# Optimization experiments

Measured on AMD Instinct MI355X. Metric: run time of the kernel, lower is better.

## Reference

```python
import jax, jax.numpy as jnp
import numpy as np

D_MODEL = 1024
N_HEADS = 16
D_FF = 4096
HEAD_DIM = D_MODEL // N_HEADS
LN_EPS = 1e-5


def layer_norm(x, g, b):
    m = jnp.mean(x, axis=-1, keepdims=True)
    v = jnp.mean(jnp.square(x - m), axis=-1, keepdims=True)
    return (x - m) * jax.lax.rsqrt(v + LN_EPS) * g + b


def setup_inputs() -> dict:
    key = jax.random.key(0)
    ks = jax.random.split(key, 16)
    s = 0.02
    d = {
        'x': jax.random.normal(ks[0], (4, 2048, D_MODEL), jnp.float32),
        'Wq': jax.random.normal(ks[1], (D_MODEL, D_MODEL), jnp.float32) * s,
        'bq': jnp.zeros((D_MODEL,), jnp.float32),
        'Wk': jax.random.normal(ks[2], (D_MODEL, D_MODEL), jnp.float32) * s,
        'bk': jnp.zeros((D_MODEL,), jnp.float32),
        'Wv': jax.random.normal(ks[3], (D_MODEL, D_MODEL), jnp.float32) * s,
        'bv': jnp.zeros((D_MODEL,), jnp.float32),
        'Wo': jax.random.normal(ks[4], (D_MODEL, D_MODEL), jnp.float32) * s,
        'bo': jnp.zeros((D_MODEL,), jnp.float32),
        'W1': jax.random.normal(ks[5], (D_FF, D_MODEL), jnp.float32) * s,
        'b1': jnp.zeros((D_FF,), jnp.float32),
        'W2': jax.random.normal(ks[6], (D_MODEL, D_FF), jnp.float32) * s,
        'b2': jnp.zeros((D_MODEL,), jnp.float32),
        'g1': jnp.ones((D_MODEL,), jnp.float32),
        'be1': jnp.zeros((D_MODEL,), jnp.float32),
        'g2': jnp.ones((D_MODEL,), jnp.float32),
        'be2': jnp.zeros((D_MODEL,), jnp.float32),
    }
    return d


def reference(x, Wq, bq, Wk, bk, Wv, bv, Wo, bo, W1, b1, W2, b2, g1, be1, g2, be2):
    B, S, D = x.shape
    H, hd = N_HEADS, HEAD_DIM
    # QKV projections; chunk along d_model -> heads (same as reshape last dim)
    q = (x @ Wq.T + bq).reshape(B, S, H, hd)
    k = (x @ Wk.T + bk).reshape(B, S, H, hd)
    v = (x @ Wv.T + bv).reshape(B, S, H, hd)
    # scaled dot-product attention (no mask, dropout = identity in eval)
    scores = jnp.einsum('bqhd,bkhd->bhqk', q, k) / jnp.sqrt(jnp.float32(hd))
    attn = jax.nn.softmax(scores, axis=-1)
    ctx = jnp.einsum('bhqk,bkhd->bqhd', attn, v).reshape(B, S, D)
    out1 = ctx @ Wo.T + bo
    out = layer_norm(x + out1, g1, be1)
    out2 = jax.nn.relu(out @ W1.T + b1) @ W2.T + b2
    # NOTE: faithful to source bug: second residual uses out1, not out
    return layer_norm(out1 + out2, g2, be2)
```

## Files before the change

kernel.cpp:

```cpp
#include <hip/hip_runtime.h>

typedef __bf16 bf16_t;
typedef __bf16 bf16x8 __attribute__((ext_vector_type(8)));
typedef __bf16 bf16x4 __attribute__((ext_vector_type(4)));
typedef float  f32x4  __attribute__((ext_vector_type(4)));

#define SEQ   2048
#define DMODEL 1024
#define DFF   4096
#define NHEAD 16
#define HDIM  64
#define MTOK  8192

#define QSCALE 0.18033688f
#define THR_LOG2 11.5f

#define MB (size_t)(1024*1024)
static const size_t XB_OFF   = 0;
static const size_t Q_OFF    = 16*MB;
static const size_t K_OFF    = 32*MB;
static const size_t VT_OFF   = 48*MB;
static const size_t FFN1_OFF = 0;
static const size_t CTX_OFF  = 64*MB;
static const size_t OUT1_OFF = 80*MB;
static const size_t LN1_OFF  = 112*MB;
static const size_t WQKV_OFF = 128*MB;
static const size_t WO_OFF   = 134*MB;
static const size_t W1_OFF   = 136*MB;
static const size_t W2_OFF   = 144*MB;

__device__ inline void gload16(const void* g, void* l) {
    __builtin_amdgcn_global_load_lds((__attribute__((address_space(1))) void*)g,
                                     (__attribute__((address_space(3))) void*)l, 16, 0, 0);
}

__global__ __launch_bounds__(256) void cast_bf16_k(const float* __restrict__ s,
                                                   bf16_t* __restrict__ d, int n8) {
    int i = blockIdx.x * 256 + threadIdx.x;
    if (i >= n8) return;
    float4 v0 = ((const float4*)s)[2*i];
    float4 v1 = ((const float4*)s)[2*i+1];
    bf16x8 o;
    o[0]=(bf16_t)v0.x; o[1]=(bf16_t)v0.y; o[2]=(bf16_t)v0.z; o[3]=(bf16_t)v0.w;
    o[4]=(bf16_t)v1.x; o[5]=(bf16_t)v1.y; o[6]=(bf16_t)v1.z; o[7]=(bf16_t)v1.w;
    *(bf16x8*)(d + (size_t)i*8) = o;
}

__global__ __launch_bounds__(256) void concat_bias_k(const float* __restrict__ a,
                                                     const float* __restrict__ b,
                                                     const float* __restrict__ c,
                                                     float* __restrict__ o) {
    int i = blockIdx.x * 256 + threadIdx.x;
    o[i] = (i < 1024) ? a[i] : ((i < 2048) ? b[i - 1024] : c[i - 2048]);
}

template<int EPI>
__global__ __launch_bounds__(256, 2) void gemm_bt(
    const bf16_t* __restrict__ A, const bf16_t* __restrict__ Bm,
    const float* __restrict__ bias, void* __restrict__ out,
    const float* __restrict__ aux, int M, int N, int K, float scale)
{
    __shared__ bf16_t As[128*64];
    __shared__ bf16_t Bs[128*64];
    const int tid = threadIdx.x;
    const int l   = tid & 63;
    const int wid = tid >> 6;
    const int wm  = wid >> 1, wn = wid & 1;
    const int c16 = l & 15,   g  = l >> 4;
    int lin = blockIdx.y * gridDim.x + blockIdx.x;
    int nwg = gridDim.x * gridDim.y;
    int swz = (lin & 7) * (nwg >> 3) + (lin >> 3);
    const long brow = (long)(swz / gridDim.x) * 128;
    const long bcol = (long)(swz % gridDim.x) * 128;

    f32x4 acc[4][4] = {};

    const int nkt = K >> 6;
    for (int kt = 0; kt < nkt; ++kt) {
        __syncthreads();
        const bf16_t* Ag = A  + brow * K + kt*64;
        const bf16_t* Bg = Bm + bcol * K + kt*64;
#pragma unroll
        for (int c = 0; c < 4; ++c) {
            int e   = (c*256 + tid) * 8;
            int row = e >> 6;
            int col = e & 63;
            gload16(Ag + (long)row*K + col, &As[e]);
            gload16(Bg + (long)row*K + col, &Bs[e]);
        }
        __syncthreads();
#pragma unroll
        for (int kk = 0; kk < 2; ++kk) {
            bf16x8 af[4], bfr[4];
#pragma unroll
            for (int mi = 0; mi < 4; ++mi)
                af[mi] = *(const bf16x8*)&As[(wm*64 + mi*16 + c16)*64 + kk*32 + 8*g];
#pragma unroll
            for (int ni = 0; ni < 4; ++ni)
                bfr[ni] = *(const bf16x8*)&Bs[(wn*64 + ni*16 + c16)*64 + kk*32 + 8*g];
#pragma unroll
            for (int mi = 0; mi < 4; ++mi)
#pragma unroll
                for (int ni = 0; ni < 4; ++ni)
                    acc[mi][ni] = __builtin_amdgcn_mfma_f32_16x16x32_bf16(
                        af[mi], bfr[ni], acc[mi][ni], 0, 0, 0);
        }
    }

#pragma unroll
    for (int ni = 0; ni < 4; ++ni) {
        const long c = bcol + wn*64 + ni*16 + c16;
        const float bv = bias[c];
#pragma unroll
        for (int mi = 0; mi < 4; ++mi) {
#pragma unroll
            for (int i = 0; i < 4; ++i) {
                const long r = brow + wm*64 + mi*16 + g*4 + i;
                float v = (acc[mi][ni][i] + bv) * scale;
                if constexpr (EPI == 2) {
                    ((float*)out)[r*N + c] = v;
                } else {
                    ((float*)out)[r*N + c] = v + aux[r*N + c];
                }
            }
        }
    }
}

template<int EPI>
__global__ __launch_bounds__(512, 2) void gemm256(
    const bf16_t* __restrict__ A, const bf16_t* __restrict__ Bm,
    const float* __restrict__ bias, void* __restrict__ out,
    void* __restrict__ out_k, void* __restrict__ out_v,
    int M, int N, int K)
{
    __shared__ alignas(16) char lds[131072];
    const int tid = threadIdx.x;
    const int l   = tid & 63;
    const int wid = tid >> 6;
    const int wm  = wid >> 2, wn = wid & 3;
    const int c16 = l & 15,   g  = l >> 4;
    const int xsw = (c16 & 7) << 4;

    int lin = blockIdx.y * gridDim.x + blockIdx.x;
    int nwg = gridDim.x * gridDim.y;
    int swz = (lin & 7) * (nwg >> 3) + (lin >> 3);
    const long brow = (long)(swz / gridDim.x) * 256;
    const long bcol = (long)(swz % gridDim.x) * 256;

    const int rowloc = tid >> 3;
    const int srcblk = (tid & 7) ^ ((tid >> 3) & 7);
    const bf16_t* Asrc = A  + (brow + rowloc) * (long)K + srcblk * 8;
    const bf16_t* Bsrc = Bm + (bcol + rowloc) * (long)K + srcblk * 8;

    f32x4 acc[8][4] = {};
    const int NKT = K >> 6;

    auto stA = [&](int cur, int t, int j) {
        gload16(Asrc + (long)j*64*K + (long)t*64, lds + cur*65536 + j*8192 + tid*16);
    };
    auto stB = [&](int cur, int t, int j) {
        gload16(Bsrc + (long)j*64*K + (long)t*64, lds + cur*65536 + 32768 + j*8192 + tid*16);
    };

#pragma unroll
    for (int j = 0; j < 4; ++j) stA(0, 0, j);
#pragma unroll
    for (int j = 0; j < 4; ++j) stB(0, 0, j);
#pragma unroll
    for (int j = 0; j < 4; ++j) stA(1, 1, j);
#pragma unroll
    for (int j = 0; j < 4; ++j) stB(1, 1, j);
    asm volatile("s_waitcnt vmcnt(8)" ::: "memory");
    __builtin_amdgcn_sched_barrier(0);
    __builtin_amdgcn_s_barrier();

    int cur = 0;
    for (int t = 0; t < NKT; ++t, cur ^= 1) {
        const char* aL = lds + cur*65536;
        const char* bL = aL + 32768;
        const bool stg = (t + 2 < NKT);
        bf16x8 a0[4][2], a1[4][2], b0[2][2], b1[2][2];

#pragma unroll
        for (int mi = 0; mi < 4; ++mi)
#pragma unroll
            for (int kk = 0; kk < 2; ++kk)
                a0[mi][kk] = *(const bf16x8*)(aL + (wm*128 + mi*16 + c16)*128 + ((kk*64 + 16*g) ^ xsw));
#pragma unroll
        for (int ni = 0; ni < 2; ++ni)
#pragma unroll
            for (int kk = 0; kk < 2; ++kk)
                b0[ni][kk] = *(const bf16x8*)(bL + (wn*64 + ni*16 + c16)*128 + ((kk*64 + 16*g) ^ xsw));
        __builtin_amdgcn_s_barrier();
        asm volatile("s_waitcnt lgkmcnt(0)" ::: "memory");
        __builtin_amdgcn_sched_barrier(0);
        __builtin_amdgcn_s_setprio(1);
#pragma unroll
        for (int mi = 0; mi < 4; ++mi)
#pragma unroll
            for (int ni = 0; ni < 2; ++ni)
#pragma unroll
                for (int kk = 0; kk < 2; ++kk)
                    acc[mi][ni] = __builtin_amdgcn_mfma_f32_16x16x32_bf16(a0[mi][kk], b0[ni][kk], acc[mi][ni], 0, 0, 0);
        __builtin_amdgcn_s_setprio(0);
        __builtin_amdgcn_s_barrier();

#pragma unroll
        for (int ni = 0; ni < 2; ++ni)
#pragma unroll
            for (int kk = 0; kk < 2; ++kk)
                b1[ni][kk] = *(const bf16x8*)(bL + (wn*64 + (ni+2)*16 + c16)*128 + ((kk*64 + 16*g) ^ xsw));
        if (stg) { stA(cur, t+2, 0); stA(cur, t+2, 2); }
        __builtin_amdgcn_s_barrier();
        asm volatile("s_waitcnt lgkmcnt(0)" ::: "memory");
        __builtin_amdgcn_sched_barrier(0);
        __builtin_amdgcn_s_setprio(1);
#pragma unroll
        for (int mi = 0; mi < 4; ++mi)
#pragma unroll
            for (int ni = 0; ni < 2; ++ni)
#pragma unroll
                for (int kk = 0; kk < 2; ++kk)
                    acc[mi][ni+2] = __builtin_amdgcn_mfma_f32_16x16x32_bf16(a0[mi][kk], b1[ni][kk], acc[mi][ni+2], 0, 0, 0);
        __builtin_amdgcn_s_setprio(0);
        __builtin_amdgcn_s_barrier();

#pragma unroll
        for (int mi = 0; mi < 4; ++mi)
#pragma unroll
            for (int kk = 0; kk < 2; ++kk)
                a1[mi][kk] = *(const bf16x8*)(aL + (wm*128 + (mi+4)*16 + c16)*128 + ((kk*64 + 16*g) ^ xsw));
        if (stg) { stB(cur, t+2, 0); stB(cur, t+2, 1); }
        __builtin_amdgcn_s_barrier();
        asm volatile("s_waitcnt lgkmcnt(0)" ::: "memory");
        __builtin_amdgcn_sched_barrier(0);
        __builtin_amdgcn_s_setprio(1);
#pragma unroll
        for (int mi = 0; mi < 4; ++mi)
#pragma unroll
            for (int ni = 0; ni < 2; ++ni)
#pragma unroll
                for (int kk = 0; kk < 2; ++kk)
                    acc[mi+4][ni] = __builtin_amdgcn_mfma_f32_16x16x32_bf16(a1[mi][kk], b0[ni][kk], acc[mi+4][ni], 0, 0, 0);
        __builtin_amdgcn_s_setprio(0);
        __builtin_amdgcn_s_barrier();

        if (stg) { stA(cur, t+2, 1); stA(cur, t+2, 3); stB(cur, t+2, 2); stB(cur, t+2, 3); }
        __builtin_amdgcn_s_barrier();
        __builtin_amdgcn_s_setprio(1);
#pragma unroll
        for (int mi = 0; mi < 4; ++mi)
#pragma unroll
            for (int ni = 0; ni < 2; ++ni)
#pragma unroll
                for (int kk = 0; kk < 2; ++kk)
                    acc[mi+4][ni+2] = __builtin_amdgcn_mfma_f32_16x16x32_bf16(a1[mi][kk], b1[ni][kk], acc[mi+4][ni+2], 0, 0, 0);
        __builtin_amdgcn_s_setprio(0);
        if (stg)                asm volatile("s_waitcnt vmcnt(8)" ::: "memory");
        else if (t < NKT - 1)   asm volatile("s_waitcnt vmcnt(0)" ::: "memory");
        __builtin_amdgcn_sched_barrier(0);
        __builtin_amdgcn_s_barrier();
    }

#pragma unroll
    for (int ni = 0; ni < 4; ++ni) {
        const long c = bcol + wn*64 + ni*16 + c16;
        const float bv = bias[c];
#pragma unroll
        for (int mi = 0; mi < 8; ++mi) {
#pragma unroll
            for (int i = 0; i < 4; ++i) {
                const long r = brow + wm*128 + mi*16 + g*4 + i;
                float v = acc[mi][ni][i] + bv;
                if constexpr (EPI == 3) {
                    ((bf16_t*)out)[r*N + c] = (bf16_t)fmaxf(v, 0.f);
                } else {
                    const int mat = (int)(c >> 10);
                    const int hc  = (int)(c & 1023);
                    const long bb = r >> 11, sidx = r & (SEQ-1);
                    const long hb = bb*NHEAD + (hc >> 6);
                    if (mat == 0)
                        ((bf16_t*)out)[(hb*SEQ + sidx)*HDIM + (hc & 63)] = (bf16_t)(v * QSCALE);
                    else if (mat == 1)
                        ((bf16_t*)out_k)[(hb*SEQ + sidx)*HDIM + (hc & 63)] = (bf16_t)v;
                    else
                        ((bf16_t*)out_v)[(hb*HDIM + (hc & 63))*SEQ + sidx] = (bf16_t)v;
                }
            }
        }
    }
}

__device__ __forceinline__ void kload(bf16x8 (&dst)[4][2], const bf16_t* kb0,
                                      int ktt, int c16, int g) {
    const bf16_t* kbase = kb0 + (size_t)ktt*64*HDIM;
#pragma unroll
    for (int jk = 0; jk < 4; ++jk)
#pragma unroll
        for (int ks = 0; ks < 2; ++ks)
            dst[jk][ks] = *(const bf16x8*)(kbase + (size_t)(16*jk + c16)*HDIM + ks*32 + 8*g);
}

__device__ __forceinline__ void vload(bf16x8 (&vr)[4][2], const bf16_t* vt0,
                                      int ktt, int c16, int g) {
#pragma unroll
    for (int nf = 0; nf < 4; ++nf)
#pragma unroll
        for (int ks = 0; ks < 2; ++ks)
            vr[nf][ks] = *(const bf16x8*)(vt0 + (size_t)(16*nf + c16)*SEQ + ktt*64 + ks*32 + 8*g);
}

__device__ __forceinline__ void qk_step(f32x4 (&s)[2][4], const bf16x8 (&kr)[4][2],
                                        const bf16x8 (&aq)[2][2]) {
    const f32x4 z = {0.f, 0.f, 0.f, 0.f};
    __builtin_amdgcn_s_setprio(1);
#pragma unroll
    for (int qf = 0; qf < 2; ++qf)
#pragma unroll
        for (int jk = 0; jk < 4; ++jk) {
            s[qf][jk] = __builtin_amdgcn_mfma_f32_16x16x32_bf16(kr[jk][0], aq[qf][0], z, 0, 0, 0);
            s[qf][jk] = __builtin_amdgcn_mfma_f32_16x16x32_bf16(kr[jk][1], aq[qf][1], s[qf][jk], 0, 0, 0);
        }
    __builtin_amdgcn_s_setprio(0);
}

__device__ __forceinline__ void sm_step(f32x4 (&s)[2][4], f32x4 (&acc)[2][4],
                                        float (&m)[2], float (&ls)[2], int g) {
#pragma unroll
    for (int qf = 0; qf < 2; ++qf) {
        f32x4 t01, t23, t03;
#pragma unroll
        for (int i = 0; i < 4; ++i) {
            t01[i] = fmaxf(s[qf][0][i], s[qf][1][i]);
            t23[i] = fmaxf(s[qf][2][i], s[qf][3][i]);
        }
#pragma unroll
        for (int i = 0; i < 4; ++i) t03[i] = fmaxf(t01[i], t23[i]);
        float lmax = fmaxf(fmaxf(t03[0], t03[1]), fmaxf(t03[2], t03[3]));
        if (__any(lmax > m[qf] + THR_LOG2)) {
            float pm = lmax;
            pm = fmaxf(pm, __shfl_xor(pm, 16, 64));
            pm = fmaxf(pm, __shfl_xor(pm, 32, 64));
            float mn   = fmaxf(m[qf], pm);
            float corr = __builtin_exp2f(m[qf] - mn);
            ls[qf] *= corr;
            m[qf]   = mn;
            float c0 = __shfl(corr, 4*g + 0, 64);
            float c1 = __shfl(corr, 4*g + 1, 64);
            float c2 = __shfl(corr, 4*g + 2, 64);
            float c3 = __shfl(corr, 4*g + 3, 64);
#pragma unroll
            for (int nf = 0; nf < 4; ++nf) {
                acc[qf][nf][0] *= c0; acc[qf][nf][1] *= c1;
                acc[qf][nf][2] *= c2; acc[qf][nf][3] *= c3;
            }
        }
#pragma unroll
        for (int jk = 0; jk < 4; ++jk)
#pragma unroll
            for (int i = 0; i < 4; ++i)
                s[qf][jk][i] = __builtin_exp2f(s[qf][jk][i] - m[qf]);
        f32x4 r01, r23, r;
#pragma unroll
        for (int i = 0; i < 4; ++i) {
            r01[i] = s[qf][0][i] + s[qf][1][i];
            r23[i] = s[qf][2][i] + s[qf][3][i];
        }
#pragma unroll
        for (int i = 0; i < 4; ++i) r[i] = r01[i] + r23[i];
        ls[qf] += (r[0] + r[1]) + (r[2] + r[3]);
    }
}

__device__ __forceinline__ void pwrite_step(const f32x4 (&s)[2][4], char* buf, int c16, int g) {
#pragma unroll
    for (int qf = 0; qf < 2; ++qf)
#pragma unroll
        for (int jk = 0; jk < 4; ++jk) {
            bf16x4 pk;
            pk[0]=(bf16_t)s[qf][jk][0]; pk[1]=(bf16_t)s[qf][jk][1];
            pk[2]=(bf16_t)s[qf][jk][2]; pk[3]=(bf16_t)s[qf][jk][3];
            *(bf16x4*)(buf + (qf*16 + c16)*128 + ((32*jk + 8*g) ^ ((c16 & 7) << 4))) = pk;
        }
}

__device__ __forceinline__ void pv_step(f32x4 (&acc)[2][4], const bf16x8 (&vr)[4][2],
                                        const char* buf, int c16, int g) {
    __builtin_amdgcn_s_setprio(1);
#pragma unroll
    for (int qf = 0; qf < 2; ++qf)
#pragma unroll
        for (int ks = 0; ks < 2; ++ks) {
            bf16x8 pa = *(const bf16x8*)(buf + (qf*16 + c16)*128 + ((ks*64 + 16*g) ^ ((c16 & 7) << 4)));
#pragma unroll
            for (int nf = 0; nf < 4; ++nf)
                acc[qf][nf] = __builtin_amdgcn_mfma_f32_16x16x32_bf16(pa, vr[nf][ks], acc[qf][nf], 0, 0, 0);
        }
    __builtin_amdgcn_s_setprio(0);
}

__global__ __launch_bounds__(256, 2) void attn_k(
    const bf16_t* __restrict__ qb, const bf16_t* __restrict__ kb,
    const bf16_t* __restrict__ vt, bf16_t* __restrict__ ctx)
{
    const int id  = blockIdx.x;
    const int idx = id >> 3;
    const int bh  = (id & 7) + 8 * (idx & 7);
    const int qt  = idx >> 3;
    const int w   = threadIdx.x >> 6;
    const int l   = threadIdx.x & 63;
    const int c16 = l & 15, g = l >> 4;
    const int q0  = qt*128 + w*32;

    __shared__ char Ps[4*8192];
    char* myP = &Ps[w*8192];

    bf16x8 aq[2][2];
#pragma unroll
    for (int qf = 0; qf < 2; ++qf) {
        const bf16_t* qrow = qb + ((size_t)bh*SEQ + q0 + qf*16 + c16)*HDIM;
        aq[qf][0] = *(const bf16x8*)(qrow + 8*g);
        aq[qf][1] = *(const bf16x8*)(qrow + 32 + 8*g);
    }

    const bf16_t* kb0 = kb + (size_t)bh*SEQ*HDIM;
    const bf16_t* vt0 = vt + (size_t)bh*HDIM*SEQ;

    f32x4 acc[2][4] = {};
    float m[2]  = {-1e30f, -1e30f};
    float ls[2] = {0.f, 0.f};

    bf16x8 kA[4][2], kB[4][2], vA[4][2], vB[4][2];
    f32x4 s[2][4];

    kload(kA, kb0, 0, c16, g);
    vload(vA, vt0, 0, c16, g);
    kload(kB, kb0, 1, c16, g);
    qk_step(s, kA, aq);
    sm_step(s, acc, m, ls, g);
    pwrite_step(s, myP, c16, g);

    const int NT = SEQ/64;
    for (int t = 0; t < NT - 2; t += 2) {
        qk_step(s, kB, aq);
        asm volatile("s_waitcnt lgkmcnt(0)" ::: "memory");
        __builtin_amdgcn_sched_barrier(0);
        kload(kA, kb0, t + 2, c16, g);
        vload(vB, vt0, t + 1, c16, g);
        __builtin_amdgcn_sched_barrier(0);
        pv_step(acc, vA, myP, c16, g);
        sm_step(s, acc, m, ls, g);
        pwrite_step(s, myP + 4096, c16, g);
        qk_step(s, kA, aq);
        asm volatile("s_waitcnt lgkmcnt(0)" ::: "memory");
        __builtin_amdgcn_sched_barrier(0);
        kload(kB, kb0, t + 3, c16, g);
        vload(vA, vt0, t + 2, c16, g);
        __builtin_amdgcn_sched_barrier(0);
        pv_step(acc, vB, myP + 4096, c16, g);
        sm_step(s, acc, m, ls, g);
        pwrite_step(s, myP, c16, g);
    }
    qk_step(s, kB, aq);
    asm volatile("s_waitcnt lgkmcnt(0)" ::: "memory");
    __builtin_amdgcn_sched_barrier(0);
    vload(vB, vt0, NT - 1, c16, g);
    __builtin_amdgcn_sched_barrier(0);
    pv_step(acc, vA, myP, c16, g);
    sm_step(s, acc, m, ls, g);
    pwrite_step(s, myP + 4096, c16, g);
    asm volatile("s_waitcnt lgkmcnt(0)" ::: "memory");
    __builtin_amdgcn_sched_barrier(0);
    pv_step(acc, vB, myP + 4096, c16, g);

    const int b = bh >> 4, h = bh & 15;
#pragma unroll
    for (int qf = 0; qf < 2; ++qf) {
        float lst = ls[qf];
        lst += __shfl_xor(lst, 16, 64);
        lst += __shfl_xor(lst, 32, 64);
        float i0 = 1.0f / __shfl(lst, 4*g + 0, 64);
        float i1 = 1.0f / __shfl(lst, 4*g + 1, 64);
        float i2 = 1.0f / __shfl(lst, 4*g + 2, 64);
        float i3 = 1.0f / __shfl(lst, 4*g + 3, 64);
#pragma unroll
        for (int nf = 0; nf < 4; ++nf) {
            long col = (size_t)h*HDIM + nf*16 + c16;
            long rb  = (size_t)b*SEQ + q0 + qf*16 + 4*g;
            ctx[(rb + 0)*DMODEL + col] = (bf16_t)(acc[qf][nf][0] * i0);
            ctx[(rb + 1)*DMODEL + col] = (bf16_t)(acc[qf][nf][1] * i1);
            ctx[(rb + 2)*DMODEL + col] = (bf16_t)(acc[qf][nf][2] * i2);
            ctx[(rb + 3)*DMODEL + col] = (bf16_t)(acc[qf][nf][3] * i3);
        }
    }
}

__global__ __launch_bounds__(256) void ln_k(
    const float* __restrict__ a, const float* __restrict__ b,
    const float* __restrict__ g, const float* __restrict__ be,
    float* __restrict__ of, bf16_t* __restrict__ ob)
{
    const long row = blockIdx.x;
    const int tid = threadIdx.x;
    float4 v = ((const float4*)(a + row*DMODEL))[tid];
    if (b) {
        float4 u = ((const float4*)(b + row*DMODEL))[tid];
        v.x += u.x; v.y += u.y; v.z += u.z; v.w += u.w;
    }
    float s = v.x + v.y + v.z + v.w;
    float q = v.x*v.x + v.y*v.y + v.z*v.z + v.w*v.w;
#pragma unroll
    for (int msk = 1; msk < 64; msk <<= 1) {
        s += __shfl_xor(s, msk, 64);
        q += __shfl_xor(q, msk, 64);
    }
    __shared__ float sb[4], qb2[4];
    int w = tid >> 6, lid = tid & 63;
    if (lid == 0) { sb[w] = s; qb2[w] = q; }
    __syncthreads();
    s = sb[0] + sb[1] + sb[2] + sb[3];
    q = qb2[0] + qb2[1] + qb2[2] + qb2[3];
    float mean = s * (1.f/1024.f);
    float var  = q * (1.f/1024.f) - mean*mean;
    float rs   = rsqrtf(var + 1e-5f);
    float4 gv = ((const float4*)g)[tid];
    float4 bv = ((const float4*)be)[tid];
    float o0 = (v.x-mean)*rs*gv.x + bv.x;
    float o1 = (v.y-mean)*rs*gv.y + bv.y;
    float o2 = (v.z-mean)*rs*gv.z + bv.z;
    float o3 = (v.w-mean)*rs*gv.w + bv.w;
    if (ob) {
        bf16x4 o; o[0]=(bf16_t)o0; o[1]=(bf16_t)o1; o[2]=(bf16_t)o2; o[3]=(bf16_t)o3;
        *(bf16x4*)(ob + row*DMODEL + tid*4) = o;
    } else {
        float4 o = make_float4(o0, o1, o2, o3);
        ((float4*)(of + row*DMODEL))[tid] = o;
    }
}

extern "C" void kernel_launch(void* const* d_in, const int* in_sizes, int n_in,
                              void* d_out, int out_size, void* d_ws, size_t ws_size,
                              hipStream_t stream)
{
    const float* x   = (const float*)d_in[0];
    const float* Wq  = (const float*)d_in[1];
    const float* bq  = (const float*)d_in[2];
    const float* Wk  = (const float*)d_in[3];
    const float* bk  = (const float*)d_in[4];
    const float* Wv  = (const float*)d_in[5];
    const float* bvv = (const float*)d_in[6];
    const float* Wo  = (const float*)d_in[7];
    const float* bo  = (const float*)d_in[8];
    const float* W1  = (const float*)d_in[9];
    const float* b1  = (const float*)d_in[10];
    const float* W2  = (const float*)d_in[11];
    const float* b2  = (const float*)d_in[12];
    const float* g1  = (const float*)d_in[13];
    const float* be1 = (const float*)d_in[14];
    const float* g2  = (const float*)d_in[15];
    const float* be2 = (const float*)d_in[16];

    char* ws = (char*)d_ws;
    bf16_t* xb   = (bf16_t*)(ws + XB_OFF);
    bf16_t* qbuf = (bf16_t*)(ws + Q_OFF);
    bf16_t* kbuf = (bf16_t*)(ws + K_OFF);
    bf16_t* vtb  = (bf16_t*)(ws + VT_OFF);
    bf16_t* ffn1 = (bf16_t*)(ws + FFN1_OFF);
    bf16_t* ctxb = (bf16_t*)(ws + CTX_OFF);
    float*  out1 = (float*)(ws + OUT1_OFF);
    bf16_t* ln1b = (bf16_t*)(ws + LN1_OFF);
    bf16_t* wqkv = (bf16_t*)(ws + WQKV_OFF);
    bf16_t* wob  = (bf16_t*)(ws + WO_OFF);
    bf16_t* w1b  = (bf16_t*)(ws + W1_OFF);
    bf16_t* w2b  = (bf16_t*)(ws + W2_OFF);
    float*  biasc= (float*)(ws + OUT1_OFF);
    float*  dout = (float*)d_out;

    auto cast = [&](const float* s, bf16_t* d, long n) {
        int n8 = (int)(n / 8);
        cast_bf16_k<<<(n8 + 255)/256, 256, 0, stream>>>(s, d, n8);
    };
    cast(x,  xb,  (long)MTOK*DMODEL);
    cast(Wq, wqkv,                        (long)DMODEL*DMODEL);
    cast(Wk, wqkv + (long)DMODEL*DMODEL,  (long)DMODEL*DMODEL);
    cast(Wv, wqkv + 2L*DMODEL*DMODEL,     (long)DMODEL*DMODEL);
    cast(Wo, wob, (long)DMODEL*DMODEL);
    cast(W1, w1b, (long)DFF*DMODEL);
    cast(W2, w2b, (long)DMODEL*DFF);
    concat_bias_k<<<12, 256, 0, stream>>>(bq, bk, bvv, biasc);

    gemm256<5><<<dim3(3*DMODEL/256, MTOK/256), dim3(512), 0, stream>>>(
        xb, wqkv, biasc, qbuf, kbuf, vtb, MTOK, 3*DMODEL, DMODEL);
    attn_k<<<dim3((SEQ/128) * 4*NHEAD), dim3(256), 0, stream>>>(qbuf, kbuf, vtb, ctxb);
    gemm_bt<2><<<dim3(DMODEL/128, MTOK/128), dim3(256), 0, stream>>>(
        ctxb, wob, bo, out1, nullptr, MTOK, DMODEL, DMODEL, 1.f);
    ln_k<<<MTOK, dim3(256), 0, stream>>>(x, out1, g1, be1, nullptr, ln1b);
    gemm256<3><<<dim3(DFF/256, MTOK/256), dim3(512), 0, stream>>>(
        ln1b, w1b, b1, ffn1, nullptr, nullptr, MTOK, DFF, DMODEL);
    gemm_bt<4><<<dim3(DMODEL/128, MTOK/128), dim3(256), 0, stream>>>(
        ffn1, w2b, b2, out1, out1, MTOK, DMODEL, DFF, 1.f);
    ln_k<<<MTOK, dim3(256), 0, stream>>>(out1, nullptr, g2, be2, dout, nullptr);
}
```

Measured before the change: 601.8 us.

## Double attention query tile per wave and restructure K/V pipeline per fragment

Each wave now processes 64 query rows, split into four 16-row fragments, instead of 32. The grid is halved to 512 blocks and the P scratch buffer in shared memory is doubled. Each loaded K/V tile is now reused across more queries, cutting global K/V traffic per query. The two-stage software pipeline with A/B register sets is replaced by a single-tile loop that interleaves per-fragment QK, softmax and P writes, and prefetches the next K tile during the last fragment. The costs are more accumulator registers, 64KB of LDS per block that may lower occupancy, fewer blocks to fill the CUs, and less overlap than the old double-buffered scheme.

```diff
diff --git a/kernel.cpp b/kernel.cpp
--- a/kernel.cpp
+++ b/kernel.cpp
@@ -311,92 +311,83 @@
             vr[nf][ks] = *(const bf16x8*)(vt0 + (size_t)(16*nf + c16)*SEQ + ktt*64 + ks*32 + 8*g);
 }
 
-__device__ __forceinline__ void qk_step(f32x4 (&s)[2][4], const bf16x8 (&kr)[4][2],
-                                        const bf16x8 (&aq)[2][2]) {
+__device__ __forceinline__ void qk1(f32x4 (&s)[4], const bf16x8 (&kr)[4][2],
+                                    const bf16x8 (&aqf)[2]) {
     const f32x4 z = {0.f, 0.f, 0.f, 0.f};
     __builtin_amdgcn_s_setprio(1);
 #pragma unroll
-    for (int qf = 0; qf < 2; ++qf)
-#pragma unroll
-        for (int jk = 0; jk < 4; ++jk) {
-            s[qf][jk] = __builtin_amdgcn_mfma_f32_16x16x32_bf16(kr[jk][0], aq[qf][0], z, 0, 0, 0);
-            s[qf][jk] = __builtin_amdgcn_mfma_f32_16x16x32_bf16(kr[jk][1], aq[qf][1], s[qf][jk], 0, 0, 0);
+    for (int jk = 0; jk < 4; ++jk) {
+        s[jk] = __builtin_amdgcn_mfma_f32_16x16x32_bf16(kr[jk][0], aqf[0], z, 0, 0, 0);
+        s[jk] = __builtin_amdgcn_mfma_f32_16x16x32_bf16(kr[jk][1], aqf[1], s[jk], 0, 0, 0);
+    }
+    __builtin_amdgcn_s_setprio(0);
+}
+
+__device__ __forceinline__ void sm1(f32x4 (&s)[4], f32x4 (&accf)[4],
+                                    float& m, float& ls, int g) {
+    f32x4 t01, t23, t03;
+#pragma unroll
+    for (int i = 0; i < 4; ++i) {
+        t01[i] = fmaxf(s[0][i], s[1][i]);
+        t23[i] = fmaxf(s[2][i], s[3][i]);
+    }
+#pragma unroll
+    for (int i = 0; i < 4; ++i) t03[i] = fmaxf(t01[i], t23[i]);
+    float lmax = fmaxf(fmaxf(t03[0], t03[1]), fmaxf(t03[2], t03[3]));
+    if (__any(lmax > m + THR_LOG2)) {
+        float pm = lmax;
+        pm = fmaxf(pm, __shfl_xor(pm, 16, 64));
+        pm = fmaxf(pm, __shfl_xor(pm, 32, 64));
+        float mn   = fmaxf(m, pm);
+        float corr = __builtin_exp2f(m - mn);
+        ls *= corr;
+        m   = mn;
+        float c0 = __shfl(corr, 4*g + 0, 64);
+        float c1 = __shfl(corr, 4*g + 1, 64);
+        float c2 = __shfl(corr, 4*g + 2, 64);
+        float c3 = __shfl(corr, 4*g + 3, 64);
+#pragma unroll
+        for (int nf = 0; nf < 4; ++nf) {
+            accf[nf][0] *= c0; accf[nf][1] *= c1;
+            accf[nf][2] *= c2; accf[nf][3] *= c3;
         }
-    __builtin_amdgcn_s_setprio(0);
-}
-
-__device__ __forceinline__ void sm_step(f32x4 (&s)[2][4], f32x4 (&acc)[2][4],
-                                        float (&m)[2], float (&ls)[2], int g) {
-#pragma unroll
-    for (int qf = 0; qf < 2; ++qf) {
-        f32x4 t01, t23, t03;
-#pragma unroll
-        for (int i = 0; i < 4; ++i) {
-            t01[i] = fmaxf(s[qf][0][i], s[qf][1][i]);
-            t23[i] = fmaxf(s[qf][2][i], s[qf][3][i]);
-        }
-#pragma unroll
-        for (int i = 0; i < 4; ++i) t03[i] = fmaxf(t01[i], t23[i]);
-        float lmax = fmaxf(fmaxf(t03[0], t03[1]), fmaxf(t03[2], t03[3]));
-        if (__any(lmax > m[qf] + THR_LOG2)) {
-            float pm = lmax;
-            pm = fmaxf(pm, __shfl_xor(pm, 16, 64));
-            pm = fmaxf(pm, __shfl_xor(pm, 32, 64));
-            float mn   = fmaxf(m[qf], pm);
-            float corr = __builtin_exp2f(m[qf] - mn);
-            ls[qf] *= corr;
-            m[qf]   = mn;
-            float c0 = __shfl(corr, 4*g + 0, 64);
-            float c1 = __shfl(corr, 4*g + 1, 64);
-            float c2 = __shfl(corr, 4*g + 2, 64);
-            float c3 = __shfl(corr, 4*g + 3, 64);
-#pragma unroll
-            for (int nf = 0; nf < 4; ++nf) {
-                acc[qf][nf][0] *= c0; acc[qf][nf][1] *= c1;
-                acc[qf][nf][2] *= c2; acc[qf][nf][3] *= c3;
-            }
-        }
-#pragma unroll
-        for (int jk = 0; jk < 4; ++jk)
-#pragma unroll
-            for (int i = 0; i < 4; ++i)
-                s[qf][jk][i] = __builtin_exp2f(s[qf][jk][i] - m[qf]);
-        f32x4 r01, r23, r;
-#pragma unroll
-        for (int i = 0; i < 4; ++i) {
-            r01[i] = s[qf][0][i] + s[qf][1][i];
-            r23[i] = s[qf][2][i] + s[qf][3][i];
-        }
-#pragma unroll
-        for (int i = 0; i < 4; ++i) r[i] = r01[i] + r23[i];
-        ls[qf] += (r[0] + r[1]) + (r[2] + r[3]);
-    }
-}
-
-__device__ __forceinline__ void pwrite_step(const f32x4 (&s)[2][4], char* buf, int c16, int g) {
-#pragma unroll
-    for (int qf = 0; qf < 2; ++qf)
-#pragma unroll
-        for (int jk = 0; jk < 4; ++jk) {
-            bf16x4 pk;
-            pk[0]=(bf16_t)s[qf][jk][0]; pk[1]=(bf16_t)s[qf][jk][1];
-            pk[2]=(bf16_t)s[qf][jk][2]; pk[3]=(bf16_t)s[qf][jk][3];
-            *(bf16x4*)(buf + (qf*16 + c16)*128 + ((32*jk + 8*g) ^ ((c16 & 7) << 4))) = pk;
-        }
-}
-
-__device__ __forceinline__ void pv_step(f32x4 (&acc)[2][4], const bf16x8 (&vr)[4][2],
-                                        const char* buf, int c16, int g) {
+    }
+#pragma unroll
+    for (int jk = 0; jk < 4; ++jk)
+#pragma unroll
+        for (int i = 0; i < 4; ++i)
+            s[jk][i] = __builtin_exp2f(s[jk][i] - m);
+    f32x4 r01, r23, r;
+#pragma unroll
+    for (int i = 0; i < 4; ++i) {
+        r01[i] = s[0][i] + s[1][i];
+        r23[i] = s[2][i] + s[3][i];
+    }
+#pragma unroll
+    for (int i = 0; i < 4; ++i) r[i] = r01[i] + r23[i];
+    ls += (r[0] + r[1]) + (r[2] + r[3]);
+}
+
+__device__ __forceinline__ void pw1(const f32x4 (&s)[4], char* buf, int qf, int c16, int g) {
+#pragma unroll
+    for (int jk = 0; jk < 4; ++jk) {
+        bf16x4 pk;
+        pk[0]=(bf16_t)s[jk][0]; pk[1]=(bf16_t)s[jk][1];
+        pk[2]=(bf16_t)s[jk][2]; pk[3]=(bf16_t)s[jk][3];
+        *(bf16x4*)(buf + (qf*16 + c16)*128 + ((32*jk + 8*g) ^ ((c16 & 7) << 4))) = pk;
+    }
+}
+
+__device__ __forceinline__ void pv1(f32x4 (&accf)[4], const bf16x8 (&vr)[4][2],
+                                    const char* buf, int qf, int c16, int g) {
     __builtin_amdgcn_s_setprio(1);
 #pragma unroll
-    for (int qf = 0; qf < 2; ++qf)
-#pragma unroll
-        for (int ks = 0; ks < 2; ++ks) {
-            bf16x8 pa = *(const bf16x8*)(buf + (qf*16 + c16)*128 + ((ks*64 + 16*g) ^ ((c16 & 7) << 4)));
-#pragma unroll
-            for (int nf = 0; nf < 4; ++nf)
-                acc[qf][nf] = __builtin_amdgcn_mfma_f32_16x16x32_bf16(pa, vr[nf][ks], acc[qf][nf], 0, 0, 0);
-        }
+    for (int ks = 0; ks < 2; ++ks) {
+        bf16x8 pa = *(const bf16x8*)(buf + (qf*16 + c16)*128 + ((ks*64 + 16*g) ^ ((c16 & 7) << 4)));
+#pragma unroll
+        for (int nf = 0; nf < 4; ++nf)
+            accf[nf] = __builtin_amdgcn_mfma_f32_16x16x32_bf16(pa, vr[nf][ks], accf[nf], 0, 0, 0);
+    }
     __builtin_amdgcn_s_setprio(0);
 }
 
@@ -411,14 +402,14 @@
     const int w   = threadIdx.x >> 6;
     const int l   = threadIdx.x & 63;
     const int c16 = l & 15, g = l >> 4;
-    const int q0  = qt*128 + w*32;
-
-    __shared__ char Ps[4*8192];
-    char* myP = &Ps[w*8192];
-
-    bf16x8 aq[2][2];
-#pragma unroll
-    for (int qf = 0; qf < 2; ++qf) {
+    const int q0  = qt*256 + w*64;
+
+    __shared__ char Ps[4*16384];
+    char* myP = &Ps[w*16384];
+
+    bf16x8 aq[4][2];
+#pragma unroll
+    for (int qf = 0; qf < 4; ++qf) {
         const bf16_t* qrow = qb + ((size_t)bh*SEQ + q0 + qf*16 + c16)*HDIM;
         aq[qf][0] = *(const bf16x8*)(qrow + 8*g);
         aq[qf][1] = *(const bf16x8*)(qrow + 32 + 8*g);
@@ -427,56 +418,38 @@
     const bf16_t* kb0 = kb + (size_t)bh*SEQ*HDIM;
     const bf16_t* vt0 = vt + (size_t)bh*HDIM*SEQ;
 
-    f32x4 acc[2][4] = {};
-    float m[2]  = {-1e30f, -1e30f};
-    float ls[2] = {0.f, 0.f};
-
-    bf16x8 kA[4][2], kB[4][2], vA[4][2], vB[4][2];
-    f32x4 s[2][4];
-
-    kload(kA, kb0, 0, c16, g);
-    vload(vA, vt0, 0, c16, g);
-    kload(kB, kb0, 1, c16, g);
-    qk_step(s, kA, aq);
-    sm_step(s, acc, m, ls, g);
-    pwrite_step(s, myP, c16, g);
+    f32x4 acc[4][4] = {};
+    float m[4]  = {-1e30f, -1e30f, -1e30f, -1e30f};
+    float ls[4] = {0.f, 0.f, 0.f, 0.f};
+
+    bf16x8 kr[4][2], vr[4][2];
+    f32x4 s[4];
+
+    kload(kr, kb0, 0, c16, g);
 
     const int NT = SEQ/64;
-    for (int t = 0; t < NT - 2; t += 2) {
-        qk_step(s, kB, aq);
+    for (int t = 0; t < NT; ++t) {
+        char* buf = myP + (t & 1) * 8192;
+        qk1(s, kr, aq[0]); sm1(s, acc[0], m[0], ls[0], g); pw1(s, buf, 0, c16, g);
+        qk1(s, kr, aq[1]); sm1(s, acc[1], m[1], ls[1], g); pw1(s, buf, 1, c16, g);
+        qk1(s, kr, aq[2]); sm1(s, acc[2], m[2], ls[2], g); pw1(s, buf, 2, c16, g);
+        qk1(s, kr, aq[3]);
+        if (t + 1 < NT) kload(kr, kb0, t + 1, c16, g);
+        vload(vr, vt0, t, c16, g);
+        __builtin_amdgcn_sched_barrier(0);
+        sm1(s, acc[3], m[3], ls[3], g); pw1(s, buf, 3, c16, g);
         asm volatile("s_waitcnt lgkmcnt(0)" ::: "memory");
         __builtin_amdgcn_sched_barrier(0);
-        kload(kA, kb0, t + 2, c16, g);
-        vload(vB, vt0, t + 1, c16, g);
-        __builtin_amdgcn_sched_barrier(0);
-        pv_step(acc, vA, myP, c16, g);
-        sm_step(s, acc, m, ls, g);
-        pwrite_step(s, myP + 4096, c16, g);
-        qk_step(s, kA, aq);
-        asm volatile("s_waitcnt lgkmcnt(0)" ::: "memory");
-        __builtin_amdgcn_sched_barrier(0);
-        kload(kB, kb0, t + 3, c16, g);
-        vload(vA, vt0, t + 2, c16, g);
-        __builtin_amdgcn_sched_barrier(0);
-        pv_step(acc, vB, myP + 4096, c16, g);
-        sm_step(s, acc, m, ls, g);
-        pwrite_step(s, myP, c16, g);
-    }
-    qk_step(s, kB, aq);
-    asm volatile("s_waitcnt lgkmcnt(0)" ::: "memory");
-    __builtin_amdgcn_sched_barrier(0);
-    vload(vB, vt0, NT - 1, c16, g);
-    __builtin_amdgcn_sched_barrier(0);
-    pv_step(acc, vA, myP, c16, g);
-    sm_step(s, acc, m, ls, g);
-    pwrite_step(s, myP + 4096, c16, g);
-    asm volatile("s_waitcnt lgkmcnt(0)" ::: "memory");
-    __builtin_amdgcn_sched_barrier(0);
-    pv_step(acc, vB, myP + 4096, c16, g);
+        pv1(acc[0], vr, buf, 0, c16, g);
+        pv1(acc[1], vr, buf, 1, c16, g);
+        pv1(acc[2], vr, buf, 2, c16, g);
+        pv1(acc[3], vr, buf, 3, c16, g);
+        asm volatile("" ::: "memory");
+    }
 
     const int b = bh >> 4, h = bh & 15;
 #pragma unroll
-    for (int qf = 0; qf < 2; ++qf) {
+    for (int qf = 0; qf < 4; ++qf) {
         float lst = ls[qf];
         lst += __shfl_xor(lst, 16, 64);
         lst += __shfl_xor(lst, 32, 64);
@@ -592,7 +565,7 @@
 
     gemm256<5><<<dim3(3*DMODEL/256, MTOK/256), dim3(512), 0, stream>>>(
         xb, wqkv, biasc, qbuf, kbuf, vtb, MTOK, 3*DMODEL, DMODEL);
-    attn_k<<<dim3((SEQ/128) * 4*NHEAD), dim3(256), 0, stream>>>(qbuf, kbuf, vtb, ctxb);
+    attn_k<<<dim3(512), dim3(256), 0, stream>>>(qbuf, kbuf, vtb, ctxb);
     gemm_bt<2><<<dim3(DMODEL/128, MTOK/128), dim3(256), 0, stream>>>(
         ctxb, wob, bo, out1, nullptr, MTOK, DMODEL, DMODEL, 1.f);
     ln_k<<<MTOK, dim3(256), 0, stream>>>(x, out1, g1, be1, nullptr, ln1b);
```

New measurement: 576.0 us. 1.04x faster.
